# Kernel optimization log

Hardware: AMD Instinct MI355X
Metric: run time of the kernel (lower is better)

The kernel has to match this reference:

```python
import jax, jax.numpy as jnp
import numpy as np

EPS = 1e-6


def setup_inputs() -> dict:
    key = jax.random.key(0)
    # (B, T, M, K, C) = (batch, time, mice, keypoints, xy)
    x = jax.random.normal(key, (64, 2048, 2, 7, 2), dtype=jnp.float32)
    return {"x": x}


def reference(x):
    B, T, M, K, C = x.shape
    P = M * K
    # --- pairwise distances over upper triangle (offset=1) ---
    flat = x.reshape(B, T, P, C)
    iu, ju = np.triu_indices(P, k=1)  # static index constants
    d = flat[:, :, iu, :] - flat[:, :, ju, :]            # (B,T,P*(P-1)/2,C)
    distances = jnp.sqrt(jnp.sum(d * d, axis=-1))        # (B,T,91)
    # --- finite-difference derivatives along time (zero-padded at t=0) ---
    zero_t = jnp.zeros_like(x[:, :1])
    v = jnp.concatenate([zero_t, x[:, 1:] - x[:, :-1]], axis=1)
    a = jnp.concatenate([zero_t, v[:, 1:] - v[:, :-1]], axis=1)
    # --- body features ---
    nose = x[..., 0, :]   # (B,T,M,2)
    neck = x[..., 3, :]
    tail = x[..., 6, :]
    body_length = jnp.linalg.norm(nose - tail, axis=-1, keepdims=True)  # (B,T,M,1)
    # NOTE: the torch code's `[..., 1:, :]` diffs over the M axis (axis=-2),
    # faithfully reproduced here.
    blc = jnp.concatenate(
        [jnp.zeros_like(body_length[:, :, :1]),
         body_length[:, :, 1:] - body_length[:, :, :-1]], axis=2)
    v1 = nose - neck
    v2 = tail - neck
    v1n = v1 / (jnp.linalg.norm(v1, axis=-1, keepdims=True) + EPS)
    v2n = v2 / (jnp.linalg.norm(v2, axis=-1, keepdims=True) + EPS)
    cos_angle = jnp.clip(jnp.sum(v1n * v2n, axis=-1, keepdims=True),
                         -1.0 + EPS, 1.0 - EPS)
    curvature = jnp.arccos(cos_angle)
    body = jnp.concatenate([body_length, blc, curvature], axis=-1).reshape(B, T, -1)
    # --- concat: raw kps + distances + velocity + acceleration + body ---
    return jnp.concatenate([
        x.reshape(B, T, -1),
        distances,
        v.reshape(B, T, -1),
        a.reshape(B, T, -1),
        body,
    ], axis=-1)
```

## Files before the change

kernel.cpp:

```cpp
#include <hip/hip_runtime.h>
#include <math.h>

#define T_DIM    2048
#define ROW_IN   28
#define ROW_OUT  181
#define EPSF     1e-6f
#define R_BLK    16
#define SLOTS    (R_BLK + 2)
#define IN_STRIDE 30
#define OUT_FLOATS (R_BLK * ROW_OUT)
#define OUT_F4     (OUT_FLOATS / 4)
#define STAGE_F4   (SLOTS * 7)
#define CVA_ITEMS  (R_BLK * 7)
#define DIST_ITEMS (R_BLK * 91)
#define BODY_ITEMS (R_BLK * 6)

typedef float vf4 __attribute__((ext_vector_type(4)));

__constant__ unsigned short d_pair[91] = {
    0x0100,0x0200,0x0300,0x0400,0x0500,0x0600,0x0700,0x0800,0x0900,0x0A00,0x0B00,0x0C00,0x0D00,
    0x0201,0x0301,0x0401,0x0501,0x0601,0x0701,0x0801,0x0901,0x0A01,0x0B01,0x0C01,0x0D01,
    0x0302,0x0402,0x0502,0x0602,0x0702,0x0802,0x0902,0x0A02,0x0B02,0x0C02,0x0D02,
    0x0403,0x0503,0x0603,0x0703,0x0803,0x0903,0x0A03,0x0B03,0x0C03,0x0D03,
    0x0504,0x0604,0x0704,0x0804,0x0904,0x0A04,0x0B04,0x0C04,0x0D04,
    0x0605,0x0705,0x0805,0x0905,0x0A05,0x0B05,0x0C05,0x0D05,
    0x0706,0x0806,0x0906,0x0A06,0x0B06,0x0C06,0x0D06,
    0x0807,0x0907,0x0A07,0x0B07,0x0C07,0x0D07,
    0x0908,0x0A08,0x0B08,0x0C08,0x0D08,
    0x0A09,0x0B09,0x0C09,0x0D09,
    0x0B0A,0x0C0A,0x0D0A,
    0x0C0B,0x0D0B,
    0x0D0C
};

__global__ __launch_bounds__(256)
void feat_kernel(const float* __restrict__ x, float* __restrict__ out)
{
    __shared__ float in_lds[SLOTS * IN_STRIDE];
    __shared__ unsigned int tbl[91];
    __shared__ float out_lds[OUT_FLOATS];

    const int tid = threadIdx.x;
    const int g0  = blockIdx.x * R_BLK;
    const vf4* __restrict__ x4 = (const vf4*)x;

    if (tid < STAGE_F4) {
        int sg = (g0 - 2) * 7 + tid;
        if (sg < 0) sg = 0;
        vf4 v = x4[sg];
        int s = tid / 7;
        int k = tid - 7 * s;
        float* dst = &in_lds[s * IN_STRIDE + 4 * k];
        ((float2*)dst)[0] = make_float2(v.x, v.y);
        ((float2*)dst)[1] = make_float2(v.z, v.w);
    } else if (tid >= 128 && tid < 128 + 91) {
        unsigned v = d_pair[tid - 128];
        tbl[tid - 128] = ((v & 0xFFu) * 8u) | (((v >> 8) * 8u) << 16);
    }

    __syncthreads();

    if (tid < CVA_ITEMS) {
        int r = tid / 7;
        int k = tid - 7 * r;
        int t = (g0 + r) & (T_DIM - 1);
        const float* cr = &in_lds[(r + 2) * IN_STRIDE + 4 * k];
        const float* pr = &in_lds[(r + 1) * IN_STRIDE + 4 * k];
        const float* qr = &in_lds[(r    ) * IN_STRIDE + 4 * k];
        float2 ca = *(const float2*)cr,  cb2 = *(const float2*)(cr + 2);
        float2 pa = *(const float2*)pr,  pb2 = *(const float2*)(pr + 2);
        float2 qa = *(const float2*)qr,  qb2 = *(const float2*)(qr + 2);
        float c[4] = {ca.x, ca.y, cb2.x, cb2.y};
        float p[4] = {pa.x, pa.y, pb2.x, pb2.y};
        float q[4] = {qa.x, qa.y, qb2.x, qb2.y};
        float* orow = &out_lds[r * ROW_OUT];
        int cb = 4 * k;
        #pragma unroll
        for (int e = 0; e < 4; ++e) {
            float v1 = c[e] - p[e];
            float a2 = c[e] - 2.0f * p[e] + q[e];
            float vv = (t >= 1) ? v1 : 0.0f;
            float aa = (t >= 2) ? a2 : ((t == 1) ? v1 : 0.0f);
            orow[cb + e]       = c[e];
            orow[119 + cb + e] = vv;
            orow[147 + cb + e] = aa;
        }
    }

    {
        const char* ldsb = (const char*)in_lds;
        #pragma unroll
        for (int it = 0; it < 6; ++it) {
            int w = tid + it * 256;
            if (it == 5 && w >= DIST_ITEMS) break;
            int r = w & (R_BLK - 1);
            int p = w >> 4;
            unsigned off = tbl[p];
            int rb = (r + 2) * (IN_STRIDE * 4);
            float2 a = *(const float2*)(ldsb + rb + (off & 0xFFFFu));
            float2 b = *(const float2*)(ldsb + rb + (off >> 16));
            float dx = a.x - b.x;
            float dy = a.y - b.y;
            out_lds[r * ROW_OUT + 28 + p] = sqrtf(dx * dx + dy * dy);
        }
    }

    if (tid < BODY_ITEMS) {
        int r   = tid & (R_BLK - 1);
        int idx = tid >> 4;
        int m   = idx >= 3 ? 1 : 0;
        int q   = idx - 3 * m;
        const float* row = &in_lds[(r + 2) * IN_STRIDE];
        const float* pr  = row + m * 14;
        float val;
        if (q == 0) {
            float dx = pr[0] - pr[12], dy = pr[1] - pr[13];
            val = sqrtf(dx * dx + dy * dy);
        } else if (q == 1) {
            if (m == 0) val = 0.0f;
            else {
                float d1x = row[14] - row[26], d1y = row[15] - row[27];
                float d0x = row[0]  - row[12], d0y = row[1]  - row[13];
                val = sqrtf(d1x*d1x + d1y*d1y) - sqrtf(d0x*d0x + d0y*d0y);
            }
        } else {
            float v1x = pr[0]  - pr[6], v1y = pr[1]  - pr[7];
            float v2x = pr[12] - pr[6], v2y = pr[13] - pr[7];
            float n1 = sqrtf(v1x*v1x + v1y*v1y) + EPSF;
            float n2 = sqrtf(v2x*v2x + v2y*v2y) + EPSF;
            float cosang = (v1x*v2x + v1y*v2y) / (n1 * n2);
            cosang = fminf(fmaxf(cosang, -1.0f + EPSF), 1.0f - EPSF);
            val = acosf(cosang);
        }
        out_lds[r * ROW_OUT + 175 + idx] = val;
    }

    __syncthreads();

    {
        const vf4* __restrict__ o4 = (const vf4*)out_lds;
        vf4* __restrict__ g4 = (vf4*)out + (size_t)blockIdx.x * OUT_F4;
        __builtin_nontemporal_store(o4[tid],       &g4[tid]);
        __builtin_nontemporal_store(o4[tid + 256], &g4[tid + 256]);
        if (tid < OUT_F4 - 512)
            __builtin_nontemporal_store(o4[tid + 512], &g4[tid + 512]);
    }
}

extern "C" void kernel_launch(void* const* d_in, const int* in_sizes, int n_in,
                              void* d_out, int out_size, void* d_ws, size_t ws_size,
                              hipStream_t stream)
{
    const float* x = (const float*)d_in[0];
    float* out = (float*)d_out;
    int n_rows = in_sizes[0] / ROW_IN;
    int grid = n_rows / R_BLK;
    feat_kernel<<<grid, 256, 0, stream>>>(x, out);
}
```

Before: 22.02 us.

## Process four row tiles per block with register prefetch of next input tile

```diff
diff --git a/kernel.cpp b/kernel.cpp
--- a/kernel.cpp
+++ b/kernel.cpp
@@ -6,6 +6,7 @@
 #define ROW_OUT  181
 #define EPSF     1e-6f
 #define R_BLK    16
+#define TILES    4
 #define SLOTS    (R_BLK + 2)
 #define IN_STRIDE 30
 #define OUT_FLOATS (R_BLK * ROW_OUT)
@@ -41,109 +42,124 @@
     __shared__ float out_lds[OUT_FLOATS];
 
     const int tid = threadIdx.x;
-    const int g0  = blockIdx.x * R_BLK;
     const vf4* __restrict__ x4 = (const vf4*)x;
 
-    if (tid < STAGE_F4) {
-        int sg = (g0 - 2) * 7 + tid;
-        if (sg < 0) sg = 0;
-        vf4 v = x4[sg];
-        int s = tid / 7;
-        int k = tid - 7 * s;
-        float* dst = &in_lds[s * IN_STRIDE + 4 * k];
-        ((float2*)dst)[0] = make_float2(v.x, v.y);
-        ((float2*)dst)[1] = make_float2(v.z, v.w);
-    } else if (tid >= 128 && tid < 128 + 91) {
-        unsigned v = d_pair[tid - 128];
-        tbl[tid - 128] = ((v & 0xFFu) * 8u) | (((v >> 8) * 8u) << 16);
+    if (tid < 91) {
+        unsigned v = d_pair[tid];
+        tbl[tid] = ((v & 0xFFu) * 8u) | (((v >> 8) * 8u) << 16);
     }
 
-    __syncthreads();
+    int tile = blockIdx.x * TILES;
+    const int s_slot = (tid < STAGE_F4) ? tid / 7 : 0;
+    const int s_k    = (tid < STAGE_F4) ? tid - 7 * s_slot : 0;
 
-    if (tid < CVA_ITEMS) {
-        int r = tid / 7;
-        int k = tid - 7 * r;
-        int t = (g0 + r) & (T_DIM - 1);
-        const float* cr = &in_lds[(r + 2) * IN_STRIDE + 4 * k];
-        const float* pr = &in_lds[(r + 1) * IN_STRIDE + 4 * k];
-        const float* qr = &in_lds[(r    ) * IN_STRIDE + 4 * k];
-        float2 ca = *(const float2*)cr,  cb2 = *(const float2*)(cr + 2);
-        float2 pa = *(const float2*)pr,  pb2 = *(const float2*)(pr + 2);
-        float2 qa = *(const float2*)qr,  qb2 = *(const float2*)(qr + 2);
-        float c[4] = {ca.x, ca.y, cb2.x, cb2.y};
-        float p[4] = {pa.x, pa.y, pb2.x, pb2.y};
-        float q[4] = {qa.x, qa.y, qb2.x, qb2.y};
-        float* orow = &out_lds[r * ROW_OUT];
-        int cb = 4 * k;
-        #pragma unroll
-        for (int e = 0; e < 4; ++e) {
-            float v1 = c[e] - p[e];
-            float a2 = c[e] - 2.0f * p[e] + q[e];
-            float vv = (t >= 1) ? v1 : 0.0f;
-            float aa = (t >= 2) ? a2 : ((t == 1) ? v1 : 0.0f);
-            orow[cb + e]       = c[e];
-            orow[119 + cb + e] = vv;
-            orow[147 + cb + e] = aa;
-        }
+    vf4 pf;
+    if (tid < STAGE_F4) {
+        int sg = (tile * R_BLK - 2) * 7 + tid;
+        if (sg < 0) sg = 0;
+        pf = x4[sg];
     }
 
-    {
-        const char* ldsb = (const char*)in_lds;
-        #pragma unroll
-        for (int it = 0; it < 6; ++it) {
-            int w = tid + it * 256;
-            if (it == 5 && w >= DIST_ITEMS) break;
-            int r = w & (R_BLK - 1);
-            int p = w >> 4;
-            unsigned off = tbl[p];
-            int rb = (r + 2) * (IN_STRIDE * 4);
-            float2 a = *(const float2*)(ldsb + rb + (off & 0xFFFFu));
-            float2 b = *(const float2*)(ldsb + rb + (off >> 16));
-            float dx = a.x - b.x;
-            float dy = a.y - b.y;
-            out_lds[r * ROW_OUT + 28 + p] = sqrtf(dx * dx + dy * dy);
+    for (int it = 0; it < TILES; ++it, ++tile) {
+        const int g0 = tile * R_BLK;
+
+        if (tid < STAGE_F4) {
+            float* dst = &in_lds[s_slot * IN_STRIDE + 4 * s_k];
+            ((float2*)dst)[0] = make_float2(pf.x, pf.y);
+            ((float2*)dst)[1] = make_float2(pf.z, pf.w);
         }
-    }
+        __syncthreads();
 
-    if (tid < BODY_ITEMS) {
-        int r   = tid & (R_BLK - 1);
-        int idx = tid >> 4;
-        int m   = idx >= 3 ? 1 : 0;
-        int q   = idx - 3 * m;
-        const float* row = &in_lds[(r + 2) * IN_STRIDE];
-        const float* pr  = row + m * 14;
-        float val;
-        if (q == 0) {
-            float dx = pr[0] - pr[12], dy = pr[1] - pr[13];
-            val = sqrtf(dx * dx + dy * dy);
-        } else if (q == 1) {
-            if (m == 0) val = 0.0f;
-            else {
-                float d1x = row[14] - row[26], d1y = row[15] - row[27];
-                float d0x = row[0]  - row[12], d0y = row[1]  - row[13];
-                val = sqrtf(d1x*d1x + d1y*d1y) - sqrtf(d0x*d0x + d0y*d0y);
+        if (tid < CVA_ITEMS) {
+            int r = tid / 7;
+            int k = tid - 7 * r;
+            int t = (g0 + r) & (T_DIM - 1);
+            const float* cr = &in_lds[(r + 2) * IN_STRIDE + 4 * k];
+            const float* pr = &in_lds[(r + 1) * IN_STRIDE + 4 * k];
+            const float* qr = &in_lds[(r    ) * IN_STRIDE + 4 * k];
+            float2 ca = *(const float2*)cr,  cb2 = *(const float2*)(cr + 2);
+            float2 pa = *(const float2*)pr,  pb2 = *(const float2*)(pr + 2);
+            float2 qa = *(const float2*)qr,  qb2 = *(const float2*)(qr + 2);
+            float c[4] = {ca.x, ca.y, cb2.x, cb2.y};
+            float p[4] = {pa.x, pa.y, pb2.x, pb2.y};
+            float q[4] = {qa.x, qa.y, qb2.x, qb2.y};
+            float* orow = &out_lds[r * ROW_OUT];
+            int cb = 4 * k;
+            #pragma unroll
+            for (int e = 0; e < 4; ++e) {
+                float v1 = c[e] - p[e];
+                float a2 = c[e] - 2.0f * p[e] + q[e];
+                float vv = (t >= 1) ? v1 : 0.0f;
+                float aa = (t >= 2) ? a2 : ((t == 1) ? v1 : 0.0f);
+                orow[cb + e]       = c[e];
+                orow[119 + cb + e] = vv;
+                orow[147 + cb + e] = aa;
             }
-        } else {
-            float v1x = pr[0]  - pr[6], v1y = pr[1]  - pr[7];
-            float v2x = pr[12] - pr[6], v2y = pr[13] - pr[7];
-            float n1 = sqrtf(v1x*v1x + v1y*v1y) + EPSF;
-            float n2 = sqrtf(v2x*v2x + v2y*v2y) + EPSF;
-            float cosang = (v1x*v2x + v1y*v2y) / (n1 * n2);
-            cosang = fminf(fmaxf(cosang, -1.0f + EPSF), 1.0f - EPSF);
-            val = acosf(cosang);
         }
-        out_lds[r * ROW_OUT + 175 + idx] = val;
-    }
 
-    __syncthreads();
+        {
+            const char* ldsb = (const char*)in_lds;
+            #pragma unroll
+            for (int itr = 0; itr < 6; ++itr) {
+                int w = tid + itr * 256;
+                if (itr == 5 && w >= DIST_ITEMS) break;
+                int r = w & (R_BLK - 1);
+                int p = w >> 4;
+                unsigned off = tbl[p];
+                int rb = (r + 2) * (IN_STRIDE * 4);
+                float2 a = *(const float2*)(ldsb + rb + (off & 0xFFFFu));
+                float2 b = *(const float2*)(ldsb + rb + (off >> 16));
+                float dx = a.x - b.x;
+                float dy = a.y - b.y;
+                out_lds[r * ROW_OUT + 28 + p] = sqrtf(dx * dx + dy * dy);
+            }
+        }
 
-    {
-        const vf4* __restrict__ o4 = (const vf4*)out_lds;
-        vf4* __restrict__ g4 = (vf4*)out + (size_t)blockIdx.x * OUT_F4;
-        __builtin_nontemporal_store(o4[tid],       &g4[tid]);
-        __builtin_nontemporal_store(o4[tid + 256], &g4[tid + 256]);
-        if (tid < OUT_F4 - 512)
-            __builtin_nontemporal_store(o4[tid + 512], &g4[tid + 512]);
+        if (tid < BODY_ITEMS) {
+            int r   = tid & (R_BLK - 1);
+            int idx = tid >> 4;
+            int m   = idx >= 3 ? 1 : 0;
+            int q   = idx - 3 * m;
+            const float* row = &in_lds[(r + 2) * IN_STRIDE];
+            const float* pr  = row + m * 14;
+            float val;
+            if (q == 0) {
+                float dx = pr[0] - pr[12], dy = pr[1] - pr[13];
+                val = sqrtf(dx * dx + dy * dy);
+            } else if (q == 1) {
+                if (m == 0) val = 0.0f;
+                else {
+                    float d1x = row[14] - row[26], d1y = row[15] - row[27];
+                    float d0x = row[0]  - row[12], d0y = row[1]  - row[13];
+                    val = sqrtf(d1x*d1x + d1y*d1y) - sqrtf(d0x*d0x + d0y*d0y);
+                }
+            } else {
+                float v1x = pr[0]  - pr[6], v1y = pr[1]  - pr[7];
+                float v2x = pr[12] - pr[6], v2y = pr[13] - pr[7];
+                float n1 = sqrtf(v1x*v1x + v1y*v1y) + EPSF;
+                float n2 = sqrtf(v2x*v2x + v2y*v2y) + EPSF;
+                float cosang = (v1x*v2x + v1y*v2y) / (n1 * n2);
+                cosang = fminf(fmaxf(cosang, -1.0f + EPSF), 1.0f - EPSF);
+                val = acosf(cosang);
+            }
+            out_lds[r * ROW_OUT + 175 + idx] = val;
+        }
+
+        if (it + 1 < TILES && tid < STAGE_F4) {
+            int sg = ((tile + 1) * R_BLK - 2) * 7 + tid;
+            pf = x4[sg];
+        }
+
+        __syncthreads();
+
+        {
+            const vf4* __restrict__ o4 = (const vf4*)out_lds;
+            vf4* __restrict__ g4 = (vf4*)out + (size_t)tile * OUT_F4;
+            __builtin_nontemporal_store(o4[tid],       &g4[tid]);
+            __builtin_nontemporal_store(o4[tid + 256], &g4[tid + 256]);
+            if (tid < OUT_F4 - 512)
+                __builtin_nontemporal_store(o4[tid + 512], &g4[tid + 512]);
+        }
     }
 }
 
@@ -154,6 +170,6 @@
     const float* x = (const float*)d_in[0];
     float* out = (float*)d_out;
     int n_rows = in_sizes[0] / ROW_IN;
-    int grid = n_rows / R_BLK;
+    int grid = n_rows / (R_BLK * TILES);
     feat_kernel<<<grid, 256, 0, stream>>>(x, out);
 }
```

Result: slower. 26.97 us (+22.5%).

## Partition rows per wave to drop the block barrier before stores

Applied to the files above, without the earlier changes.

```diff
diff --git a/kernel.cpp b/kernel.cpp
--- a/kernel.cpp
+++ b/kernel.cpp
@@ -10,10 +10,9 @@
 #define IN_STRIDE 30
 #define OUT_FLOATS (R_BLK * ROW_OUT)
 #define OUT_F4     (OUT_FLOATS / 4)
+#define WAVE_F4    (OUT_F4 / 4)
 #define STAGE_F4   (SLOTS * 7)
-#define CVA_ITEMS  (R_BLK * 7)
-#define DIST_ITEMS (R_BLK * 91)
-#define BODY_ITEMS (R_BLK * 6)
+#define DIST_WAVE  (4 * 91)
 
 typedef float vf4 __attribute__((ext_vector_type(4)));
 
@@ -40,8 +39,10 @@
     __shared__ unsigned int tbl[91];
     __shared__ float out_lds[OUT_FLOATS];
 
-    const int tid = threadIdx.x;
-    const int g0  = blockIdx.x * R_BLK;
+    const int tid  = threadIdx.x;
+    const int lane = tid & 63;
+    const int wv   = tid >> 6;
+    const int g0   = blockIdx.x * R_BLK;
     const vf4* __restrict__ x4 = (const vf4*)x;
 
     if (tid < STAGE_F4) {
@@ -60,9 +61,11 @@
 
     __syncthreads();
 
-    if (tid < CVA_ITEMS) {
-        int r = tid / 7;
-        int k = tid - 7 * r;
+    const int r0 = 4 * wv;
+
+    if (lane < 28) {
+        int r = r0 + (lane & 3);
+        int k = lane >> 2;
         int t = (g0 + r) & (T_DIM - 1);
         const float* cr = &in_lds[(r + 2) * IN_STRIDE + 4 * k];
         const float* pr = &in_lds[(r + 1) * IN_STRIDE + 4 * k];
@@ -90,11 +93,11 @@
     {
         const char* ldsb = (const char*)in_lds;
         #pragma unroll
-        for (int it = 0; it < 6; ++it) {
-            int w = tid + it * 256;
-            if (it == 5 && w >= DIST_ITEMS) break;
-            int r = w & (R_BLK - 1);
-            int p = w >> 4;
+        for (int kk = 0; kk < 6; ++kk) {
+            int it = lane + 64 * kk;
+            if (kk == 5 && it >= DIST_WAVE) break;
+            int r = r0 + (it & 3);
+            int p = it >> 2;
             unsigned off = tbl[p];
             int rb = (r + 2) * (IN_STRIDE * 4);
             float2 a = *(const float2*)(ldsb + rb + (off & 0xFFFFu));
@@ -105,9 +108,9 @@
         }
     }
 
-    if (tid < BODY_ITEMS) {
-        int r   = tid & (R_BLK - 1);
-        int idx = tid >> 4;
+    if (lane < 24) {
+        int r   = r0 + (lane & 3);
+        int idx = lane >> 2;
         int m   = idx >= 3 ? 1 : 0;
         int q   = idx - 3 * m;
         const float* row = &in_lds[(r + 2) * IN_STRIDE];
@@ -135,15 +138,13 @@
         out_lds[r * ROW_OUT + 175 + idx] = val;
     }
 
-    __syncthreads();
-
     {
-        const vf4* __restrict__ o4 = (const vf4*)out_lds;
-        vf4* __restrict__ g4 = (vf4*)out + (size_t)blockIdx.x * OUT_F4;
-        __builtin_nontemporal_store(o4[tid],       &g4[tid]);
-        __builtin_nontemporal_store(o4[tid + 256], &g4[tid + 256]);
-        if (tid < OUT_F4 - 512)
-            __builtin_nontemporal_store(o4[tid + 512], &g4[tid + 512]);
+        const vf4* __restrict__ o4 = (const vf4*)out_lds + wv * WAVE_F4;
+        vf4* __restrict__ g4 = (vf4*)out + (size_t)blockIdx.x * OUT_F4 + wv * WAVE_F4;
+        __builtin_nontemporal_store(o4[lane],      &g4[lane]);
+        __builtin_nontemporal_store(o4[lane + 64], &g4[lane + 64]);
+        if (lane < WAVE_F4 - 128)
+            __builtin_nontemporal_store(o4[lane + 128], &g4[lane + 128]);
     }
 }
 
```

Result: slower. 23.81 us (+8.1%).
